# Performance work log

Measured on AMD Instinct MI355X. Metric: run time of the kernel, lower is better.

## Reference

```python
import jax, jax.numpy as jnp
import numpy as np

SR = 16000
NYQ = SR / 2.0
N_FFT = 400
HOP = 160
WIN = 400
OUT_CHANNELS = 64
OUTPUT_SIZE = 64
MIN_LOW_HZ = 50.0
MIN_BAND_HZ = 50.0
FRAME_LENGTH = 400
EPS_LN = 1e-5


def _to_mel(hz):
    return 2595.0 * np.log10(1.0 + hz / 700.0)


def _to_hz(mel):
    return 700.0 * (10.0 ** (mel / 2595.0) - 1.0)


def setup_inputs() -> dict:
    key = jax.random.key(0)
    k1, = jax.random.split(key, 1)
    waveforms = jax.random.normal(k1, (1024, 1, 16000), dtype=jnp.float32)
    # mel-spaced init, exactly as in __init__ (freq_init='mel', range_constraint=False)
    low_hz = 30.0
    high_hz = NYQ - (MIN_LOW_HZ + MIN_BAND_HZ)
    mel = np.linspace(_to_mel(low_hz), _to_mel(high_hz), OUT_CHANNELS + 1)
    hz = _to_hz(mel)
    low_hz_ = jnp.asarray(hz[:-1], dtype=jnp.float32).reshape(-1, 1)
    band_hz_ = jnp.asarray(np.diff(hz), dtype=jnp.float32).reshape(-1, 1)
    ln_weight = jnp.ones((OUT_CHANNELS, 1), dtype=jnp.float32)
    ln_bias = jnp.zeros((OUT_CHANNELS, 1), dtype=jnp.float32)
    return {
        "waveforms": waveforms,
        "low_hz_": low_hz_,
        "band_hz_": band_hz_,
        "ln_weight": ln_weight,
        "ln_bias": ln_bias,
    }


def _hann_periodic(n):
    # torch.hann_window default: periodic=True
    k = jnp.arange(n, dtype=jnp.float32)
    return 0.5 - 0.5 * jnp.cos(2.0 * jnp.pi * k / n)


def _stft_mag(x):
    pad = N_FFT // 2
    xp = jnp.pad(x, ((0, 0), (pad, pad)), mode="reflect")
    n_frames = 1 + (xp.shape[1] - N_FFT) // HOP
    idx = jnp.arange(n_frames)[:, None] * HOP + jnp.arange(N_FFT)[None, :]
    frames = xp[:, idx] * _hann_periodic(WIN)  # [B, F_t, n_fft]
    spec = jnp.fft.rfft(frames, axis=-1)       # [B, F_t, n_fft//2+1]
    return jnp.abs(spec).transpose(0, 2, 1)    # [B, n_fft//2+1, F_t]


def _get_filters(low_hz_, band_hz_):
    # vectorized over all channels (original loops per channel)
    low = MIN_LOW_HZ + jnp.abs(low_hz_)                                   # [C,1]
    high = jnp.clip(low + MIN_BAND_HZ + jnp.abs(band_hz_), MIN_LOW_HZ, NYQ)
    freq = jnp.linspace(0.0, NYQ, N_FFT // 2 + 1, dtype=jnp.float32)      # [F]
    mask = (freq >= low) & (freq <= high)                                 # [C,F]
    center = (low + high) / 2.0
    bw = high - low
    resp = 1.0 - jnp.abs(freq - center) / (bw / 2.0)                      # triangular
    return jnp.where(mask, resp, 0.0)                                     # [C,F]


def _gln(x, weight, bias):
    # GlobalLayerNorm over dims (1,2) of [B,C,T]
    mean = jnp.mean(x, axis=(1, 2), keepdims=True)
    var = jnp.mean((x - mean) ** 2, axis=(1, 2), keepdims=True)
    return weight * (x - mean) / jnp.sqrt(var + EPS_LN) + bias


def _interp_linear(x, out_size):
    # torch F.interpolate(mode='linear', align_corners=False) along last dim
    t_in = x.shape[-1]
    scale = t_in / out_size
    pos = (jnp.arange(out_size, dtype=jnp.float32) + 0.5) * scale - 0.5
    pos = jnp.clip(pos, 0.0, t_in - 1)
    i0 = jnp.floor(pos).astype(jnp.int32)
    i1 = jnp.minimum(i0 + 1, t_in - 1)
    w = (pos - i0.astype(jnp.float32))
    return x[..., i0] * (1.0 - w) + x[..., i1] * w


def reference(waveforms, low_hz_, band_hz_, ln_weight, ln_bias):
    B = waveforms.shape[0]
    target_length = HOP * (OUTPUT_SIZE - 1) + FRAME_LENGTH  # 10480
    cur = waveforms.shape[-1]
    x = waveforms[:, 0, :]
    if target_length > cur:  # static shape decision
        x = jnp.pad(x, ((0, 0), (0, target_length - cur)))
    mag_spec = _stft_mag(x)                       # [B, 201, F_t]
    filters = _get_filters(low_hz_, band_hz_)     # [C, 201]
    filtered = jnp.einsum("cf,bft->bct", filters, mag_spec)  # [B, C, F_t]
    filtered = _gln(filtered, ln_weight, ln_bias)
    energy = filtered ** 2
    log_energy = jnp.log10(energy + 1e-6)         # [B, C, F_t]
    if log_energy.shape[-1] != OUTPUT_SIZE:
        log_energy = _interp_linear(log_energy, OUTPUT_SIZE)  # [B, C, 64]
    log_energy = log_energy[:, None, :, :].transpose(0, 1, 3, 2)  # [B,1,64,C]
    return (log_energy, filters)
```

## Files before the change

### kernel.cpp

```cpp
#include <hip/hip_runtime.h>
#include <math.h>

#define BLOCK 512
#define MSTR 209

typedef __attribute__((ext_vector_type(8))) short short8;
typedef __attribute__((ext_vector_type(16))) float f32x16;
typedef __attribute__((ext_vector_type(8))) float f32x8;

__device__ inline unsigned short f2bf(float x) {
    unsigned u = __float_as_uint(x);
    unsigned r = u + 0x7fffu + ((u >> 16) & 1u);
    return (unsigned short)(r >> 16);
}

struct ASplit { short8 h, l; };

__device__ inline ASplit splitA(f32x8 v) {
    unsigned ah[4], al[4];
    #pragma unroll
    for (int q = 0; q < 4; ++q) {
        unsigned short h0 = f2bf(v[2*q]),   h1 = f2bf(v[2*q+1]);
        float hf0 = __uint_as_float((unsigned)h0 << 16);
        float hf1 = __uint_as_float((unsigned)h1 << 16);
        unsigned short l0 = f2bf(v[2*q] - hf0), l1 = f2bf(v[2*q+1] - hf1);
        ah[q] = (unsigned)h0 | ((unsigned)h1 << 16);
        al[q] = (unsigned)l0 | ((unsigned)l1 << 16);
    }
    ASplit r;
    r.h = __builtin_bit_cast(short8, *(uint4*)ah);
    r.l = __builtin_bit_cast(short8, *(uint4*)al);
    return r;
}

__device__ inline f32x8 loadA8(const float* __restrict__ x, int i0) {
    f32x8 r;
    if (i0 >= 0 && i0 <= 15992) {
        float4 a0 = *(const float4*)(x + i0);
        float4 a1 = *(const float4*)(x + i0 + 4);
        r[0] = a0.x; r[1] = a0.y; r[2] = a0.z; r[3] = a0.w;
        r[4] = a1.x; r[5] = a1.y; r[6] = a1.z; r[7] = a1.w;
    } else {
        #pragma unroll
        for (int e = 0; e < 8; ++e) {
            int p = i0 + e;
            p = (p < 0) ? -p : p;
            p = (p > 15999) ? (31998 - p) : p;
            r[e] = x[p];
        }
    }
    return r;
}

__global__ void fse_filters(const float* __restrict__ low_hz_,
                            const float* __restrict__ band_hz_,
                            float* __restrict__ out)
{
    int idx = blockIdx.x * 256 + threadIdx.x;
    if (idx >= 64 * 201) return;
    int c = idx / 201;
    int k = idx - c * 201;
    float lo = 50.0f + fabsf(low_hz_[c]);
    float hi = lo + 50.0f + fabsf(band_hz_[c]);
    hi = fminf(fmaxf(hi, 50.0f), 8000.0f);
    float ctr = 0.5f * (lo + hi);
    float hbw = 0.5f * (hi - lo);
    float fq = 40.0f * (float)k;
    float resp = 1.0f - fabsf(fq - ctr) / hbw;
    out[idx] = (fq >= lo && fq <= hi) ? resp : 0.0f;
}

__global__ void fse_setup_B(unsigned short* __restrict__ bt)
{
    int idx = blockIdx.x * 256 + threadIdx.x;
    if (idx >= 372736) return;
    int e   = idx & 7;
    int t   = idx >> 3;
    int row = t % 448;
    int q   = t / 448;
    int p   = q & 3;
    int pl  = (q >> 2) & 1;
    int kc  = q >> 3;
    int n   = kc * 32 + p * 8 + e;
    float v = 0.0f;
    if (n < 400) {
        int bin = -1, isim = 0;
        if (row <= 200) bin = row;
        else if (row >= 224 && row <= 424) { bin = row - 224; isim = 1; }
        if (bin >= 0) {
            int a = (bin * n) % 400;
            float th = 6.283185307179586f * ((float)a / 400.0f);
            float sn, cs;
            sincosf(th, &sn, &cs);
            float wn = 0.5f - 0.5f * cosf(6.283185307179586f * ((float)n / 400.0f));
            v = isim ? (-wn * sn) : (wn * cs);
        }
    }
    unsigned short h = f2bf(v);
    float hf = __uint_as_float((unsigned)h << 16);
    unsigned short l = f2bf(v - hf);
    bt[idx] = pl ? l : h;
}

__global__ __launch_bounds__(512, 2)
void fse_main_mfma(const float* __restrict__ wav,
                   const float* __restrict__ low_hz_,
                   const float* __restrict__ band_hz_,
                   const float* __restrict__ ln_w,
                   const float* __restrict__ ln_b,
                   const unsigned short* __restrict__ Bt,
                   float* __restrict__ out)
{
    __shared__ __align__(16) char smem[114688];
    float* mags = (float*)smem;
    float* fbuf = (float*)(smem + 84544);

    __shared__ float fctr[64], finv[64];
    __shared__ int   fks[64], fke[64];
    __shared__ float red[16];
    __shared__ float stats[2];

    const int b    = blockIdx.x;
    const int tid  = threadIdx.x;
    const int w    = tid >> 6;
    const int lane = tid & 63;
    const float* __restrict__ x = wav + b * 16000;

    if (tid < 64) {
        float lo = 50.0f + fabsf(low_hz_[tid]);
        float hi = lo + 50.0f + fabsf(band_hz_[tid]);
        hi = fminf(fmaxf(hi, 50.0f), 8000.0f);
        float ctr = 0.5f * (lo + hi);
        float hbw = 0.5f * (hi - lo);
        int ks = (int)ceilf(lo * 0.025f);
        if (ks < 0) ks = 0;
        while (40.0f * (float)ks < lo) ++ks;
        while (ks > 0 && 40.0f * (float)(ks - 1) >= lo) --ks;
        int ke = (int)floorf(hi * 0.025f);
        if (ke > 200) ke = 200;
        while (40.0f * (float)ke > hi) --ke;
        while (ke < 200 && 40.0f * (float)(ke + 1) <= hi) ++ke;
        fctr[tid] = ctr;
        finv[tid] = (hbw > 0.0f) ? (1.0f / hbw) : 0.0f;
        fks[tid]  = ks;
        fke[tid]  = ke;
    }

    const int mt   = w >> 1;
    const int half = w & 1;
    const int jrow = lane & 31;
    const int g    = lane >> 5;
    const int arow = mt * 32 + jrow;
    const int te   = (arow <= 100) ? arow : 50;
    const int abase = 160 * te - 200 + g * 8;

    const uint4* __restrict__ btg = (const uint4*)Bt;

    f32x8 ac0 = loadA8(x, abase);
    f32x8 ac1 = loadA8(x, abase + 16);
    {
        uint4 rr0 = btg[0 * 512 + tid], rr1 = btg[1 * 512 + tid];
        uint4 rr2 = btg[2 * 512 + tid], rr3 = btg[3 * 512 + tid];
        uint4 rr4 = btg[4 * 512 + tid], rr5 = btg[5 * 512 + tid];
        uint4 rr6 = btg[6 * 512 + tid];
        uint4* dst = (uint4*)smem;
        dst[0 * 512 + tid] = rr0; dst[1 * 512 + tid] = rr1;
        dst[2 * 512 + tid] = rr2; dst[3 * 512 + tid] = rr3;
        dst[4 * 512 + tid] = rr4; dst[5 * 512 + tid] = rr5;
        dst[6 * 512 + tid] = rr6;
    }
    __syncthreads();

    f32x16 acc[7];
    #pragma unroll
    for (int n = 0; n < 7; ++n) {
        #pragma unroll
        for (int e = 0; e < 16; ++e) acc[n][e] = 0.0f;
    }

    int curoff = 0;
    for (int kc = 0; kc < 13; ++kc) {
        const bool pre = (kc < 12);
        uint4 rr0, rr1, rr2, rr3, rr4, rr5, rr6;
        f32x8 an0, an1;
        if (pre) {
            const uint4* src = btg + (kc + 1) * 3584;
            rr0 = src[0 * 512 + tid]; rr1 = src[1 * 512 + tid];
            rr2 = src[2 * 512 + tid]; rr3 = src[3 * 512 + tid];
            rr4 = src[4 * 512 + tid]; rr5 = src[5 * 512 + tid];
            rr6 = src[6 * 512 + tid];
            an0 = loadA8(x, abase + (kc + 1) * 32);
            an1 = loadA8(x, abase + (kc + 1) * 32 + 16);
        }

        ASplit A0 = splitA(ac0);
        ASplit A1 = splitA(ac1);

        const unsigned short* bs = (const unsigned short*)(smem + curoff);
        #pragma unroll
        for (int s = 0; s < 2; ++s) {
            const short8 Ah = s ? A1.h : A0.h;
            const short8 Al = s ? A1.l : A0.l;
            const int pb = (s * 2 + g) * 448;
            #pragma unroll
            for (int n = 0; n < 7; ++n) {
                const int ro = (half * 7 + n) * 32 + jrow;
                short8 Bh = *(const short8*)(bs + (pb + ro) * 8);
                short8 Bl = *(const short8*)(bs + 14336 + (pb + ro) * 8);
                acc[n] = __builtin_amdgcn_mfma_f32_32x32x16_bf16(Ah, Bh, acc[n], 0, 0, 0);
                acc[n] = __builtin_amdgcn_mfma_f32_32x32x16_bf16(Ah, Bl, acc[n], 0, 0, 0);
                acc[n] = __builtin_amdgcn_mfma_f32_32x32x16_bf16(Al, Bh, acc[n], 0, 0, 0);
            }
        }

        if (pre) {
            uint4* dst = (uint4*)(smem + (curoff ^ 57344));
            dst[0 * 512 + tid] = rr0; dst[1 * 512 + tid] = rr1;
            dst[2 * 512 + tid] = rr2; dst[3 * 512 + tid] = rr3;
            dst[4 * 512 + tid] = rr4; dst[5 * 512 + tid] = rr5;
            dst[6 * 512 + tid] = rr6;
        }
        __syncthreads();
        if (pre) { ac0 = an0; ac1 = an1; }
        curoff ^= 57344;
    }

    if (half == 0) {
        #pragma unroll
        for (int n = 0; n < 7; ++n) {
            int k = n * 32 + jrow;
            if (k <= 200) {
                #pragma unroll
                for (int r = 0; r < 16; ++r) {
                    int t = mt * 32 + (r & 3) + 8 * (r >> 2) + 4 * g;
                    if (t <= 100) mags[t * MSTR + k] = acc[n][r];
                }
            }
        }
    }
    __syncthreads();
    if (half == 1) {
        #pragma unroll
        for (int n = 0; n < 7; ++n) {
            int k = n * 32 + jrow;
            if (k <= 200) {
                #pragma unroll
                for (int r = 0; r < 16; ++r) {
                    int t = mt * 32 + (r & 3) + 8 * (r >> 2) + 4 * g;
                    if (t <= 100) {
                        float re = mags[t * MSTR + k];
                        float im = acc[n][r];
                        mags[t * MSTR + k] = sqrtf(re * re + im * im);
                    }
                }
            }
        }
    }
    __syncthreads();

    {
        const int t0 = lane;
        const int t1v = 64 + lane;
        const int t1 = (t1v <= 100) ? t1v : 100;
        #pragma unroll
        for (int i = 0; i < 8; ++i) {
            const int c = w * 8 + i;
            const float ctr = fctr[c];
            const float inv = finv[c];
            const int ks = fks[c], ke = fke[c];
            float a0 = 0.0f, a1 = 0.0f;
            for (int k = ks; k <= ke; ++k) {
                float resp = 1.0f - fabsf(40.0f * (float)k - ctr) * inv;
                a0 = fmaf(resp, mags[t0 * MSTR + k], a0);
                a1 = fmaf(resp, mags[t1 * MSTR + k], a1);
            }
            fbuf[c * 101 + t0] = a0;
            if (t1v <= 100) fbuf[c * 101 + t1v] = a1;
        }
    }
    __syncthreads();

    float s = 0.0f, ss = 0.0f;
    for (int i = tid; i < 6464; i += BLOCK) {
        float vv = fbuf[i];
        s += vv;
        ss = fmaf(vv, vv, ss);
    }
    #pragma unroll
    for (int off = 32; off > 0; off >>= 1) {
        s  += __shfl_down(s,  off, 64);
        ss += __shfl_down(ss, off, 64);
    }
    if (lane == 0) { red[w] = s; red[8 + w] = ss; }
    __syncthreads();
    if (tid == 0) {
        float ts = 0.0f, tss = 0.0f;
        for (int i = 0; i < 8; ++i) { ts += red[i]; tss += red[8 + i]; }
        float mu = ts * (1.0f / 6464.0f);
        stats[0] = mu;
        stats[1] = tss * (1.0f / 6464.0f) - mu * mu;
    }
    __syncthreads();
    const float mu   = stats[0];
    const float isig = 1.0f / sqrtf(stats[1] + 1e-5f);

    for (int idx = tid; idx < 4096; idx += BLOCK) {
        const int to = idx >> 6;
        const int c  = idx & 63;
        float pos = ((float)to + 0.5f) * 1.578125f - 0.5f;
        pos = fminf(fmaxf(pos, 0.0f), 100.0f);
        int i0 = (int)floorf(pos);
        int i1 = i0 + 1; if (i1 > 100) i1 = 100;
        float fr = pos - (float)i0;
        float wc = ln_w[c], bc = ln_b[c];
        float x0 = fbuf[c * 101 + i0];
        float x1 = fbuf[c * 101 + i1];
        float y0 = fmaf(wc, (x0 - mu) * isig, bc);
        float y1 = fmaf(wc, (x1 - mu) * isig, bc);
        float l0 = log10f(fmaf(y0, y0, 1e-6f));
        float l1 = log10f(fmaf(y1, y1, 1e-6f));
        out[b * 4096 + idx] = l0 * (1.0f - fr) + l1 * fr;
    }
}

__global__ __launch_bounds__(512, 2)
void fse_main_valu(const float* __restrict__ wav,
                   const float* __restrict__ low_hz_,
                   const float* __restrict__ band_hz_,
                   const float* __restrict__ ln_w,
                   const float* __restrict__ ln_b,
                   float* __restrict__ out)
{
    __shared__ float  xp[16400];
    __shared__ float2 Xs[8][204];
    __shared__ float  mags[8][204];
    __shared__ float  fbuf[64 * 101];
    __shared__ float  fctr[64], finv[64];
    __shared__ int    fks[64], fke[64];
    __shared__ float  red[8];
    __shared__ float  stats[2];

    const int b    = blockIdx.x;
    const int tid  = threadIdx.x;
    const int w    = tid >> 6;
    const int lane = tid & 63;
    const float* __restrict__ x = wav + b * 16000;

    for (int i = tid; i < 16400; i += BLOCK) {
        int p = i - 200;
        p = (p < 0) ? -p : p;
        p = (p > 15999) ? (31998 - p) : p;
        xp[i] = x[p];
    }
    if (tid < 64) {
        float lo = 50.0f + fabsf(low_hz_[tid]);
        float hi = lo + 50.0f + fabsf(band_hz_[tid]);
        hi = fminf(fmaxf(hi, 50.0f), 8000.0f);
        float ctr = 0.5f * (lo + hi);
        float hbw = 0.5f * (hi - lo);
        int ks = (int)ceilf(lo * 0.025f);
        if (ks < 0) ks = 0;
        while (40.0f * (float)ks < lo) ++ks;
        while (ks > 0 && 40.0f * (float)(ks - 1) >= lo) --ks;
        int ke = (int)floorf(hi * 0.025f);
        if (ke > 200) ke = 200;
        while (40.0f * (float)ke > hi) --ke;
        while (ke < 200 && 40.0f * (float)(ke + 1) <= hi) ++ke;
        fctr[tid] = ctr;
        finv[tid] = (hbw > 0.0f) ? (1.0f / hbw) : 0.0f;
        fks[tid]  = ks;
        fke[tid]  = ke;
    }
    __syncthreads();

    const float cctr = fctr[lane];
    const float cinv = finv[lane];
    const int   cks  = fks[lane];
    const int   cke  = fke[lane];

    float reX[4][13], imX[4][13];
    const float2* __restrict__ xp2 = (const float2*)xp;
    float c0[4], s0[4], c1[4], s1[4], cd[4], sd[4];
    #pragma unroll
    for (int m = 0; m < 4; ++m) {
        const int k = m * 64 + lane;
        const float th = -0.015707963267948966f * (float)k;
        sincosf(th, &s1[m], &c1[m]);
        sincosf(th + th, &sd[m], &cd[m]);
        c0[m] = 1.0f; s0[m] = 0.0f;
        #pragma unroll
        for (int j = 0; j < 13; ++j) { reX[m][j] = 0.0f; imX[m][j] = 0.0f; }
    }
    const int o12 = (w < 5) ? 640 * 12 : 0;
    int ib = 80 * w;
    #pragma unroll 2
    for (int h = 0; h < 200; ++h) {
        #pragma unroll
        for (int j = 0; j < 13; ++j) {
            const int off = (j == 12) ? o12 : 640 * j;
            float2 f = xp2[ib + off];
            #pragma unroll
            for (int m = 0; m < 4; ++m) {
                reX[m][j] = fmaf(f.x, c0[m], reX[m][j]);
                imX[m][j] = fmaf(f.x, s0[m], imX[m][j]);
                reX[m][j] = fmaf(f.y, c1[m], reX[m][j]);
                imX[m][j] = fmaf(f.y, s1[m], imX[m][j]);
            }
        }
        #pragma unroll
        for (int m = 0; m < 4; ++m) {
            float nc0 = fmaf(c0[m], cd[m], -(s0[m] * sd[m]));
            float ns0 = fmaf(s0[m], cd[m],  (c0[m] * sd[m]));
            float nc1 = fmaf(c1[m], cd[m], -(s1[m] * sd[m]));
            float ns1 = fmaf(s1[m], cd[m],  (c1[m] * sd[m]));
            c0[m] = nc0; s0[m] = ns0; c1[m] = nc1; s1[m] = ns1;
        }
        ++ib;
    }

    float2* __restrict__ myX   = &Xs[w][0];
    float*  __restrict__ mymag = &mags[w][0];
    for (int j = 0; j < 13; ++j) {
        const int t = w + 8 * j;
        if (t > 100) break;
        #pragma unroll
        for (int m = 0; m < 4; ++m) {
            const int k = m * 64 + lane;
            if (k < 202) myX[k] = make_float2(reX[m][j], imX[m][j]);
        }
        asm volatile("s_waitcnt lgkmcnt(0)" ::: "memory");
        #pragma unroll
        for (int m = 0; m < 4; ++m) {
            const int k = m * 64 + lane;
            if (k <= 200) {
                float2 xm = (k == 0) ? myX[1] : myX[k - 1];
                float imm = (k == 0) ? -xm.y : xm.y;
                float2 xq = myX[k + 1];
                float rw = 0.5f * reX[m][j] - 0.25f * (xm.x + xq.x);
                float iw = 0.5f * imX[m][j] - 0.25f * (imm  + xq.y);
                mymag[k] = sqrtf(rw * rw + iw * iw);
            }
        }
        asm volatile("s_waitcnt lgkmcnt(0)" ::: "memory");
        float acc = 0.0f;
        for (int k = cks; k <= cke; ++k) {
            float resp = 1.0f - fabsf(40.0f * (float)k - cctr) * cinv;
            acc = fmaf(resp, mymag[k], acc);
        }
        fbuf[lane * 101 + t] = acc;
    }
    __syncthreads();

    float s = 0.0f;
    for (int i = tid; i < 6464; i += BLOCK) s += fbuf[i];
    #pragma unroll
    for (int off = 32; off > 0; off >>= 1) s += __shfl_down(s, off, 64);
    if (lane == 0) red[w] = s;
    __syncthreads();
    if (tid == 0) {
        float tsum = 0.0f;
        for (int i = 0; i < 8; ++i) tsum += red[i];
        stats[0] = tsum * (1.0f / 6464.0f);
    }
    __syncthreads();
    const float mu = stats[0];
    float v = 0.0f;
    for (int i = tid; i < 6464; i += BLOCK) { float d = fbuf[i] - mu; v = fmaf(d, d, v); }
    #pragma unroll
    for (int off = 32; off > 0; off >>= 1) v += __shfl_down(v, off, 64);
    if (lane == 0) red[w] = v;
    __syncthreads();
    if (tid == 0) {
        float tsum = 0.0f;
        for (int i = 0; i < 8; ++i) tsum += red[i];
        stats[1] = tsum * (1.0f / 6464.0f);
    }
    __syncthreads();
    const float var  = stats[1];
    const float isig = 1.0f / sqrtf(var + 1e-5f);

    for (int idx = tid; idx < 4096; idx += BLOCK) {
        const int to = idx >> 6;
        const int c  = idx & 63;
        float pos = ((float)to + 0.5f) * 1.578125f - 0.5f;
        pos = fminf(fmaxf(pos, 0.0f), 100.0f);
        int i0 = (int)floorf(pos);
        int i1 = i0 + 1; if (i1 > 100) i1 = 100;
        float fr = pos - (float)i0;
        float wc = ln_w[c], bc = ln_b[c];
        float x0 = fbuf[c * 101 + i0];
        float x1 = fbuf[c * 101 + i1];
        float y0 = fmaf(wc, (x0 - mu) * isig, bc);
        float y1 = fmaf(wc, (x1 - mu) * isig, bc);
        float l0 = log10f(fmaf(y0, y0, 1e-6f));
        float l1 = log10f(fmaf(y1, y1, 1e-6f));
        out[b * 4096 + idx] = l0 * (1.0f - fr) + l1 * fr;
    }
}

extern "C" void kernel_launch(void* const* d_in, const int* in_sizes, int n_in,
                              void* d_out, int out_size, void* d_ws, size_t ws_size,
                              hipStream_t stream)
{
    const float* wav = (const float*)d_in[0];
    const float* lo  = (const float*)d_in[1];
    const float* bd  = (const float*)d_in[2];
    const float* lw  = (const float*)d_in[3];
    const float* lb  = (const float*)d_in[4];
    float* out = (float*)d_out;

    fse_filters<<<(64 * 201 + 255) / 256, 256, 0, stream>>>(lo, bd, out + 1024 * 4096);

    const size_t BNEED = (size_t)372736 * sizeof(unsigned short);
    if (ws_size >= BNEED) {
        unsigned short* Bts = (unsigned short*)d_ws;
        fse_setup_B<<<(372736 + 255) / 256, 256, 0, stream>>>(Bts);
        fse_main_mfma<<<1024, BLOCK, 0, stream>>>(wav, lo, bd, lw, lb, Bts, out);
    } else {
        fse_main_valu<<<1024, BLOCK, 0, stream>>>(wav, lo, bd, lw, lb, out);
    }
}
```

Baseline: 231.7 us.

## Split fused STFT kernel into per-half-batch GEMM kernel and separate layernorm kernel

The single per-batch fused kernel becomes two kernels. A GEMM kernel runs two blocks per batch element, each covering half the time frames, stages B tiles into LDS with global_load_lds instead of register-staged double buffering, computes real and imaginary parts in the same wave so magnitude needs no LDS round trip, and writes filtered energies to workspace. A second kernel then does layernorm, log, and interpolation. The aim is to raise occupancy (lower LDS per block, 4 blocks per CU) and parallelism, at the cost of an extra global round trip for the intermediate, an extra launch, and dropping the prefetch overlap. The VALU fallback path is removed, and the fused MFMA kernel is kept as the fallback when workspace is small.

Result: slower. 249.7 us (+7.8%).

```diff
diff --git a/kernel.cpp b/kernel.cpp
--- a/kernel.cpp
+++ b/kernel.cpp
@@ -1,8 +1,5 @@
 #include <hip/hip_runtime.h>
 #include <math.h>
-
-#define BLOCK 512
-#define MSTR 209
 
 typedef __attribute__((ext_vector_type(8))) short short8;
 typedef __attribute__((ext_vector_type(16))) float f32x16;
@@ -50,6 +47,27 @@
         }
     }
     return r;
+}
+
+__device__ inline void filter_params(int c, const float* low_hz_, const float* band_hz_,
+                                     float* fctr, float* finv, int* fks, int* fke) {
+    float lo = 50.0f + fabsf(low_hz_[c]);
+    float hi = lo + 50.0f + fabsf(band_hz_[c]);
+    hi = fminf(fmaxf(hi, 50.0f), 8000.0f);
+    float ctr = 0.5f * (lo + hi);
+    float hbw = 0.5f * (hi - lo);
+    int ks = (int)ceilf(lo * 0.025f);
+    if (ks < 0) ks = 0;
+    while (40.0f * (float)ks < lo) ++ks;
+    while (ks > 0 && 40.0f * (float)(ks - 1) >= lo) --ks;
+    int ke = (int)floorf(hi * 0.025f);
+    if (ke > 200) ke = 200;
+    while (40.0f * (float)ke > hi) --ke;
+    while (ke < 200 && 40.0f * (float)(ke + 1) <= hi) ++ke;
+    fctr[c] = ctr;
+    finv[c] = (hbw > 0.0f) ? (1.0f / hbw) : 0.0f;
+    fks[c]  = ks;
+    fke[c]  = ke;
 }
 
 __global__ void fse_filters(const float* __restrict__ low_hz_,
@@ -102,200 +120,158 @@
     bt[idx] = pl ? l : h;
 }
 
-__global__ __launch_bounds__(512, 2)
-void fse_main_mfma(const float* __restrict__ wav,
-                   const float* __restrict__ low_hz_,
-                   const float* __restrict__ band_hz_,
-                   const float* __restrict__ ln_w,
-                   const float* __restrict__ ln_b,
-                   const unsigned short* __restrict__ Bt,
-                   float* __restrict__ out)
+__global__ __launch_bounds__(512, 4)
+void fse_gemm(const float* __restrict__ wav,
+              const float* __restrict__ low_hz_,
+              const float* __restrict__ band_hz_,
+              const unsigned short* __restrict__ Bt,
+              float* __restrict__ filt)
 {
-    __shared__ __align__(16) char smem[114688];
-    float* mags = (float*)smem;
-    float* fbuf = (float*)(smem + 84544);
-
+    __shared__ __align__(16) char smem[57344];
     __shared__ float fctr[64], finv[64];
     __shared__ int   fks[64], fke[64];
-    __shared__ float red[16];
+    float* mags = (float*)smem;
+
+    const int bid  = blockIdx.x;
+    const int b    = bid >> 1;
+    const int half = bid & 1;
+    const int tid  = threadIdx.x;
+    const int w    = tid >> 6;
+    const int lane = tid & 63;
+    const float* __restrict__ x = wav + b * 16000;
+
+    if (tid < 64) filter_params(tid, low_hz_, band_hz_, fctr, finv, fks, fke);
+
+    const int mt    = w >> 2;
+    const int pq    = w & 3;
+    const int pbase = pq * 2;
+    const int cnt   = (pq < 3) ? 2 : 1;
+    const int jrow  = lane & 31;
+    const int g     = lane >> 5;
+
+    const int arow = 64 * half + 32 * mt + jrow;
+    const int te   = (arow <= 100) ? arow : 50;
+    const int ab   = 160 * te - 200 + g * 8;
+
+    f32x16 accR[2], accI[2];
+    #pragma unroll
+    for (int i = 0; i < 2; ++i)
+        #pragma unroll
+        for (int e = 0; e < 16; ++e) { accR[i][e] = 0.0f; accI[i][e] = 0.0f; }
+
+    for (int kc = 0; kc < 13; ++kc) {
+        __syncthreads();
+        {
+            const uint4* src = (const uint4*)Bt + kc * 3584 + (w << 6) + lane;
+            char* dstb = smem + (w << 6) * 16;
+            #pragma unroll
+            for (int i = 0; i < 7; ++i) {
+                __builtin_amdgcn_global_load_lds(
+                    (const __attribute__((address_space(1))) unsigned*)(src + i * 512),
+                    (__attribute__((address_space(3))) unsigned*)(dstb + i * 8192),
+                    16, 0, 0);
+            }
+        }
+        __syncthreads();
+
+        f32x8 a0 = loadA8(x, ab + kc * 32);
+        f32x8 a1 = loadA8(x, ab + kc * 32 + 16);
+
+        const unsigned short* bs = (const unsigned short*)smem;
+        #pragma unroll
+        for (int s = 0; s < 2; ++s) {
+            ASplit S = splitA(s ? a1 : a0);
+            const int part = s * 2 + g;
+            const int bhof = part * 3584;
+            const int blof = (4 + part) * 3584;
+            #pragma unroll
+            for (int i = 0; i < 2; ++i) {
+                if (i < cnt) {
+                    const int p = pbase + i;
+                    const int roR = p * 32 + jrow;
+                    const int roI = (p + 7) * 32 + jrow;
+                    short8 BhR = *(const short8*)(bs + bhof + roR * 8);
+                    short8 BlR = *(const short8*)(bs + blof + roR * 8);
+                    short8 BhI = *(const short8*)(bs + bhof + roI * 8);
+                    short8 BlI = *(const short8*)(bs + blof + roI * 8);
+                    accR[i] = __builtin_amdgcn_mfma_f32_32x32x16_bf16(S.h, BhR, accR[i], 0, 0, 0);
+                    accR[i] = __builtin_amdgcn_mfma_f32_32x32x16_bf16(S.h, BlR, accR[i], 0, 0, 0);
+                    accR[i] = __builtin_amdgcn_mfma_f32_32x32x16_bf16(S.l, BhR, accR[i], 0, 0, 0);
+                    accI[i] = __builtin_amdgcn_mfma_f32_32x32x16_bf16(S.h, BhI, accI[i], 0, 0, 0);
+                    accI[i] = __builtin_amdgcn_mfma_f32_32x32x16_bf16(S.h, BlI, accI[i], 0, 0, 0);
+                    accI[i] = __builtin_amdgcn_mfma_f32_32x32x16_bf16(S.l, BhI, accI[i], 0, 0, 0);
+                }
+            }
+        }
+    }
+
+    __syncthreads();
+
+    #pragma unroll
+    for (int i = 0; i < 2; ++i) {
+        if (i < cnt) {
+            const int k = (pbase + i) * 32 + jrow;
+            if (k <= 200) {
+                #pragma unroll
+                for (int r = 0; r < 16; ++r) {
+                    int tl = 32 * mt + (r & 3) + 8 * (r >> 2) + 4 * g;
+                    float re = accR[i][r];
+                    float im = accI[i][r];
+                    mags[tl * 201 + k] = sqrtf(re * re + im * im);
+                }
+            }
+        }
+    }
+    __syncthreads();
+
+    const int tg = 64 * half + lane;
+    #pragma unroll
+    for (int i = 0; i < 8; ++i) {
+        const int c = w * 8 + i;
+        const float ctr = fctr[c];
+        const float inv = finv[c];
+        const int ks = fks[c], ke = fke[c];
+        float a = 0.0f;
+        for (int k = ks; k <= ke; ++k) {
+            float resp = 1.0f - fabsf(40.0f * (float)k - ctr) * inv;
+            a = fmaf(resp, mags[lane * 201 + k], a);
+        }
+        if (tg <= 100) filt[b * 6464 + c * 101 + tg] = a;
+    }
+}
+
+__global__ __launch_bounds__(256)
+void fse_post(const float* __restrict__ filt,
+              const float* __restrict__ ln_w,
+              const float* __restrict__ ln_b,
+              float* __restrict__ out)
+{
+    __shared__ float fbuf[6464];
+    __shared__ float red[8];
     __shared__ float stats[2];
-
     const int b    = blockIdx.x;
     const int tid  = threadIdx.x;
     const int w    = tid >> 6;
     const int lane = tid & 63;
-    const float* __restrict__ x = wav + b * 16000;
-
-    if (tid < 64) {
-        float lo = 50.0f + fabsf(low_hz_[tid]);
-        float hi = lo + 50.0f + fabsf(band_hz_[tid]);
-        hi = fminf(fmaxf(hi, 50.0f), 8000.0f);
-        float ctr = 0.5f * (lo + hi);
-        float hbw = 0.5f * (hi - lo);
-        int ks = (int)ceilf(lo * 0.025f);
-        if (ks < 0) ks = 0;
-        while (40.0f * (float)ks < lo) ++ks;
-        while (ks > 0 && 40.0f * (float)(ks - 1) >= lo) --ks;
-        int ke = (int)floorf(hi * 0.025f);
-        if (ke > 200) ke = 200;
-        while (40.0f * (float)ke > hi) --ke;
-        while (ke < 200 && 40.0f * (float)(ke + 1) <= hi) ++ke;
-        fctr[tid] = ctr;
-        finv[tid] = (hbw > 0.0f) ? (1.0f / hbw) : 0.0f;
-        fks[tid]  = ks;
-        fke[tid]  = ke;
-    }
-
-    const int mt   = w >> 1;
-    const int half = w & 1;
-    const int jrow = lane & 31;
-    const int g    = lane >> 5;
-    const int arow = mt * 32 + jrow;
-    const int te   = (arow <= 100) ? arow : 50;
-    const int abase = 160 * te - 200 + g * 8;
-
-    const uint4* __restrict__ btg = (const uint4*)Bt;
-
-    f32x8 ac0 = loadA8(x, abase);
-    f32x8 ac1 = loadA8(x, abase + 16);
-    {
-        uint4 rr0 = btg[0 * 512 + tid], rr1 = btg[1 * 512 + tid];
-        uint4 rr2 = btg[2 * 512 + tid], rr3 = btg[3 * 512 + tid];
-        uint4 rr4 = btg[4 * 512 + tid], rr5 = btg[5 * 512 + tid];
-        uint4 rr6 = btg[6 * 512 + tid];
-        uint4* dst = (uint4*)smem;
-        dst[0 * 512 + tid] = rr0; dst[1 * 512 + tid] = rr1;
-        dst[2 * 512 + tid] = rr2; dst[3 * 512 + tid] = rr3;
-        dst[4 * 512 + tid] = rr4; dst[5 * 512 + tid] = rr5;
-        dst[6 * 512 + tid] = rr6;
-    }
-    __syncthreads();
-
-    f32x16 acc[7];
-    #pragma unroll
-    for (int n = 0; n < 7; ++n) {
-        #pragma unroll
-        for (int e = 0; e < 16; ++e) acc[n][e] = 0.0f;
-    }
-
-    int curoff = 0;
-    for (int kc = 0; kc < 13; ++kc) {
-        const bool pre = (kc < 12);
-        uint4 rr0, rr1, rr2, rr3, rr4, rr5, rr6;
-        f32x8 an0, an1;
-        if (pre) {
-            const uint4* src = btg + (kc + 1) * 3584;
-            rr0 = src[0 * 512 + tid]; rr1 = src[1 * 512 + tid];
-            rr2 = src[2 * 512 + tid]; rr3 = src[3 * 512 + tid];
-            rr4 = src[4 * 512 + tid]; rr5 = src[5 * 512 + tid];
-            rr6 = src[6 * 512 + tid];
-            an0 = loadA8(x, abase + (kc + 1) * 32);
-            an1 = loadA8(x, abase + (kc + 1) * 32 + 16);
-        }
-
-        ASplit A0 = splitA(ac0);
-        ASplit A1 = splitA(ac1);
-
-        const unsigned short* bs = (const unsigned short*)(smem + curoff);
-        #pragma unroll
-        for (int s = 0; s < 2; ++s) {
-            const short8 Ah = s ? A1.h : A0.h;
-            const short8 Al = s ? A1.l : A0.l;
-            const int pb = (s * 2 + g) * 448;
-            #pragma unroll
-            for (int n = 0; n < 7; ++n) {
-                const int ro = (half * 7 + n) * 32 + jrow;
-                short8 Bh = *(const short8*)(bs + (pb + ro) * 8);
-                short8 Bl = *(const short8*)(bs + 14336 + (pb + ro) * 8);
-                acc[n] = __builtin_amdgcn_mfma_f32_32x32x16_bf16(Ah, Bh, acc[n], 0, 0, 0);
-                acc[n] = __builtin_amdgcn_mfma_f32_32x32x16_bf16(Ah, Bl, acc[n], 0, 0, 0);
-                acc[n] = __builtin_amdgcn_mfma_f32_32x32x16_bf16(Al, Bh, acc[n], 0, 0, 0);
-            }
-        }
-
-        if (pre) {
-            uint4* dst = (uint4*)(smem + (curoff ^ 57344));
-            dst[0 * 512 + tid] = rr0; dst[1 * 512 + tid] = rr1;
-            dst[2 * 512 + tid] = rr2; dst[3 * 512 + tid] = rr3;
-            dst[4 * 512 + tid] = rr4; dst[5 * 512 + tid] = rr5;
-            dst[6 * 512 + tid] = rr6;
-        }
-        __syncthreads();
-        if (pre) { ac0 = an0; ac1 = an1; }
-        curoff ^= 57344;
-    }
-
-    if (half == 0) {
-        #pragma unroll
-        for (int n = 0; n < 7; ++n) {
-            int k = n * 32 + jrow;
-            if (k <= 200) {
-                #pragma unroll
-                for (int r = 0; r < 16; ++r) {
-                    int t = mt * 32 + (r & 3) + 8 * (r >> 2) + 4 * g;
-                    if (t <= 100) mags[t * MSTR + k] = acc[n][r];
-                }
-            }
-        }
-    }
-    __syncthreads();
-    if (half == 1) {
-        #pragma unroll
-        for (int n = 0; n < 7; ++n) {
-            int k = n * 32 + jrow;
-            if (k <= 200) {
-                #pragma unroll
-                for (int r = 0; r < 16; ++r) {
-                    int t = mt * 32 + (r & 3) + 8 * (r >> 2) + 4 * g;
-                    if (t <= 100) {
-                        float re = mags[t * MSTR + k];
-                        float im = acc[n][r];
-                        mags[t * MSTR + k] = sqrtf(re * re + im * im);
-                    }
-                }
-            }
-        }
-    }
-    __syncthreads();
-
-    {
-        const int t0 = lane;
-        const int t1v = 64 + lane;
-        const int t1 = (t1v <= 100) ? t1v : 100;
-        #pragma unroll
-        for (int i = 0; i < 8; ++i) {
-            const int c = w * 8 + i;
-            const float ctr = fctr[c];
-            const float inv = finv[c];
-            const int ks = fks[c], ke = fke[c];
-            float a0 = 0.0f, a1 = 0.0f;
-            for (int k = ks; k <= ke; ++k) {
-                float resp = 1.0f - fabsf(40.0f * (float)k - ctr) * inv;
-                a0 = fmaf(resp, mags[t0 * MSTR + k], a0);
-                a1 = fmaf(resp, mags[t1 * MSTR + k], a1);
-            }
-            fbuf[c * 101 + t0] = a0;
-            if (t1v <= 100) fbuf[c * 101 + t1v] = a1;
-        }
-    }
-    __syncthreads();
+    const float* __restrict__ src = filt + b * 6464;
 
     float s = 0.0f, ss = 0.0f;
-    for (int i = tid; i < 6464; i += BLOCK) {
-        float vv = fbuf[i];
-        s += vv;
-        ss = fmaf(vv, vv, ss);
+    for (int i = tid; i < 6464; i += 256) {
+        float v = src[i];
+        fbuf[i] = v;
+        s += v;
+        ss = fmaf(v, v, ss);
     }
     #pragma unroll
     for (int off = 32; off > 0; off >>= 1) {
         s  += __shfl_down(s,  off, 64);
         ss += __shfl_down(ss, off, 64);
     }
-    if (lane == 0) { red[w] = s; red[8 + w] = ss; }
+    if (lane == 0) { red[w] = s; red[4 + w] = ss; }
     __syncthreads();
     if (tid == 0) {
         float ts = 0.0f, tss = 0.0f;
-        for (int i = 0; i < 8; ++i) { ts += red[i]; tss += red[8 + i]; }
+        for (int i = 0; i < 4; ++i) { ts += red[i]; tss += red[4 + i]; }
         float mu = ts * (1.0f / 6464.0f);
         stats[0] = mu;
         stats[1] = tss * (1.0f / 6464.0f) - mu * mu;
@@ -304,7 +280,7 @@
     const float mu   = stats[0];
     const float isig = 1.0f / sqrtf(stats[1] + 1e-5f);
 
-    for (int idx = tid; idx < 4096; idx += BLOCK) {
+    for (int idx = tid; idx < 4096; idx += 256) {
         const int to = idx >> 6;
         const int c  = idx & 63;
         float pos = ((float)to + 0.5f) * 1.578125f - 0.5f;
@@ -323,22 +299,23 @@
     }
 }
 
+#define MSTR 209
 __global__ __launch_bounds__(512, 2)
-void fse_main_valu(const float* __restrict__ wav,
-                   const float* __restrict__ low_hz_,
-                   const float* __restrict__ band_hz_,
-                   const float* __restrict__ ln_w,
-                   const float* __restrict__ ln_b,
-                   float* __restrict__ out)
+void fse_main_fused(const float* __restrict__ wav,
+                    const float* __restrict__ low_hz_,
+                    const float* __restrict__ band_hz_,
+                    const float* __restrict__ ln_w,
+                    const float* __restrict__ ln_b,
+                    const unsigned short* __restrict__ Bt,
+                    float* __restrict__ out)
 {
-    __shared__ float  xp[16400];
-    __shared__ float2 Xs[8][204];
-    __shared__ float  mags[8][204];
-    __shared__ float  fbuf[64 * 101];
-    __shared__ float  fctr[64], finv[64];
-    __shared__ int    fks[64], fke[64];
-    __shared__ float  red[8];
-    __shared__ float  stats[2];
+    __shared__ __align__(16) char smem[114688];
+    float* mags = (float*)smem;
+    float* fbuf = (float*)(smem + 84544);
+    __shared__ float fctr[64], finv[64];
+    __shared__ int   fks[64], fke[64];
+    __shared__ float red[16];
+    __shared__ float stats[2];
 
     const int b    = blockIdx.x;
     const int tid  = threadIdx.x;
@@ -346,140 +323,164 @@
     const int lane = tid & 63;
     const float* __restrict__ x = wav + b * 16000;
 
-    for (int i = tid; i < 16400; i += BLOCK) {
-        int p = i - 200;
-        p = (p < 0) ? -p : p;
-        p = (p > 15999) ? (31998 - p) : p;
-        xp[i] = x[p];
-    }
-    if (tid < 64) {
-        float lo = 50.0f + fabsf(low_hz_[tid]);
-        float hi = lo + 50.0f + fabsf(band_hz_[tid]);
-        hi = fminf(fmaxf(hi, 50.0f), 8000.0f);
-        float ctr = 0.5f * (lo + hi);
-        float hbw = 0.5f * (hi - lo);
-        int ks = (int)ceilf(lo * 0.025f);
-        if (ks < 0) ks = 0;
-        while (40.0f * (float)ks < lo) ++ks;
-        while (ks > 0 && 40.0f * (float)(ks - 1) >= lo) --ks;
-        int ke = (int)floorf(hi * 0.025f);
-        if (ke > 200) ke = 200;
-        while (40.0f * (float)ke > hi) --ke;
-        while (ke < 200 && 40.0f * (float)(ke + 1) <= hi) ++ke;
-        fctr[tid] = ctr;
-        finv[tid] = (hbw > 0.0f) ? (1.0f / hbw) : 0.0f;
-        fks[tid]  = ks;
-        fke[tid]  = ke;
-    }
-    __syncthreads();
-
-    const float cctr = fctr[lane];
-    const float cinv = finv[lane];
-    const int   cks  = fks[lane];
-    const int   cke  = fke[lane];
-
-    float reX[4][13], imX[4][13];
-    const float2* __restrict__ xp2 = (const float2*)xp;
-    float c0[4], s0[4], c1[4], s1[4], cd[4], sd[4];
-    #pragma unroll
-    for (int m = 0; m < 4; ++m) {
-        const int k = m * 64 + lane;
-        const float th = -0.015707963267948966f * (float)k;
-        sincosf(th, &s1[m], &c1[m]);
-        sincosf(th + th, &sd[m], &cd[m]);
-        c0[m] = 1.0f; s0[m] = 0.0f;
-        #pragma unroll
-        for (int j = 0; j < 13; ++j) { reX[m][j] = 0.0f; imX[m][j] = 0.0f; }
-    }
-    const int o12 = (w < 5) ? 640 * 12 : 0;
-    int ib = 80 * w;
-    #pragma unroll 2
-    for (int h = 0; h < 200; ++h) {
-        #pragma unroll
-        for (int j = 0; j < 13; ++j) {
-            const int off = (j == 12) ? o12 : 640 * j;
-            float2 f = xp2[ib + off];
+    if (tid < 64) filter_params(tid, low_hz_, band_hz_, fctr, finv, fks, fke);
+
+    const int mt   = w >> 1;
+    const int half = w & 1;
+    const int jrow = lane & 31;
+    const int g    = lane >> 5;
+    const int arow = mt * 32 + jrow;
+    const int te   = (arow <= 100) ? arow : 50;
+    const int abase = 160 * te - 200 + g * 8;
+
+    const uint4* __restrict__ btg = (const uint4*)Bt;
+
+    f32x8 ac0 = loadA8(x, abase);
+    f32x8 ac1 = loadA8(x, abase + 16);
+    {
+        uint4 rr0 = btg[0 * 512 + tid], rr1 = btg[1 * 512 + tid];
+        uint4 rr2 = btg[2 * 512 + tid], rr3 = btg[3 * 512 + tid];
+        uint4 rr4 = btg[4 * 512 + tid], rr5 = btg[5 * 512 + tid];
+        uint4 rr6 = btg[6 * 512 + tid];
+        uint4* dst = (uint4*)smem;
+        dst[0 * 512 + tid] = rr0; dst[1 * 512 + tid] = rr1;
+        dst[2 * 512 + tid] = rr2; dst[3 * 512 + tid] = rr3;
+        dst[4 * 512 + tid] = rr4; dst[5 * 512 + tid] = rr5;
+        dst[6 * 512 + tid] = rr6;
+    }
+    __syncthreads();
+
+    f32x16 acc[7];
+    #pragma unroll
+    for (int n = 0; n < 7; ++n)
+        #pragma unroll
+        for (int e = 0; e < 16; ++e) acc[n][e] = 0.0f;
+
+    int curoff = 0;
+    for (int kc = 0; kc < 13; ++kc) {
+        const bool pre = (kc < 12);
+        uint4 rr0, rr1, rr2, rr3, rr4, rr5, rr6;
+        f32x8 an0, an1;
+        if (pre) {
+            const uint4* src = btg + (kc + 1) * 3584;
+            rr0 = src[0 * 512 + tid]; rr1 = src[1 * 512 + tid];
+            rr2 = src[2 * 512 + tid]; rr3 = src[3 * 512 + tid];
+            rr4 = src[4 * 512 + tid]; rr5 = src[5 * 512 + tid];
+            rr6 = src[6 * 512 + tid];
+            an0 = loadA8(x, abase + (kc + 1) * 32);
+            an1 = loadA8(x, abase + (kc + 1) * 32 + 16);
+        }
+        ASplit A0 = splitA(ac0);
+        ASplit A1 = splitA(ac1);
+
+        const unsigned short* bs = (const unsigned short*)(smem + curoff);
+        #pragma unroll
+        for (int s = 0; s < 2; ++s) {
+            const short8 Ah = s ? A1.h : A0.h;
+            const short8 Al = s ? A1.l : A0.l;
+            const int pb = (s * 2 + g) * 448;
             #pragma unroll
-            for (int m = 0; m < 4; ++m) {
-                reX[m][j] = fmaf(f.x, c0[m], reX[m][j]);
-                imX[m][j] = fmaf(f.x, s0[m], imX[m][j]);
-                reX[m][j] = fmaf(f.y, c1[m], reX[m][j]);
-                imX[m][j] = fmaf(f.y, s1[m], imX[m][j]);
-            }
-        }
-        #pragma unroll
-        for (int m = 0; m < 4; ++m) {
-            float nc0 = fmaf(c0[m], cd[m], -(s0[m] * sd[m]));
-            float ns0 = fmaf(s0[m], cd[m],  (c0[m] * sd[m]));
-            float nc1 = fmaf(c1[m], cd[m], -(s1[m] * sd[m]));
-            float ns1 = fmaf(s1[m], cd[m],  (c1[m] * sd[m]));
-            c0[m] = nc0; s0[m] = ns0; c1[m] = nc1; s1[m] = ns1;
-        }
-        ++ib;
-    }
-
-    float2* __restrict__ myX   = &Xs[w][0];
-    float*  __restrict__ mymag = &mags[w][0];
-    for (int j = 0; j < 13; ++j) {
-        const int t = w + 8 * j;
-        if (t > 100) break;
-        #pragma unroll
-        for (int m = 0; m < 4; ++m) {
-            const int k = m * 64 + lane;
-            if (k < 202) myX[k] = make_float2(reX[m][j], imX[m][j]);
-        }
-        asm volatile("s_waitcnt lgkmcnt(0)" ::: "memory");
-        #pragma unroll
-        for (int m = 0; m < 4; ++m) {
-            const int k = m * 64 + lane;
+            for (int n = 0; n < 7; ++n) {
+                const int ro = (half * 7 + n) * 32 + jrow;
+                short8 Bh = *(const short8*)(bs + (pb + ro) * 8);
+                short8 Bl = *(const short8*)(bs + 14336 + (pb + ro) * 8);
+                acc[n] = __builtin_amdgcn_mfma_f32_32x32x16_bf16(Ah, Bh, acc[n], 0, 0, 0);
+                acc[n] = __builtin_amdgcn_mfma_f32_32x32x16_bf16(Ah, Bl, acc[n], 0, 0, 0);
+                acc[n] = __builtin_amdgcn_mfma_f32_32x32x16_bf16(Al, Bh, acc[n], 0, 0, 0);
+            }
+        }
+        if (pre) {
+            uint4* dst = (uint4*)(smem + (curoff ^ 57344));
+            dst[0 * 512 + tid] = rr0; dst[1 * 512 + tid] = rr1;
+            dst[2 * 512 + tid] = rr2; dst[3 * 512 + tid] = rr3;
+            dst[4 * 512 + tid] = rr4; dst[5 * 512 + tid] = rr5;
+            dst[6 * 512 + tid] = rr6;
+        }
+        __syncthreads();
+        if (pre) { ac0 = an0; ac1 = an1; }
+        curoff ^= 57344;
+    }
+
+    if (half == 0) {
+        #pragma unroll
+        for (int n = 0; n < 7; ++n) {
+            int k = n * 32 + jrow;
             if (k <= 200) {
-                float2 xm = (k == 0) ? myX[1] : myX[k - 1];
-                float imm = (k == 0) ? -xm.y : xm.y;
-                float2 xq = myX[k + 1];
-                float rw = 0.5f * reX[m][j] - 0.25f * (xm.x + xq.x);
-                float iw = 0.5f * imX[m][j] - 0.25f * (imm  + xq.y);
-                mymag[k] = sqrtf(rw * rw + iw * iw);
-            }
-        }
-        asm volatile("s_waitcnt lgkmcnt(0)" ::: "memory");
-        float acc = 0.0f;
-        for (int k = cks; k <= cke; ++k) {
-            float resp = 1.0f - fabsf(40.0f * (float)k - cctr) * cinv;
-            acc = fmaf(resp, mymag[k], acc);
-        }
-        fbuf[lane * 101 + t] = acc;
-    }
-    __syncthreads();
-
-    float s = 0.0f;
-    for (int i = tid; i < 6464; i += BLOCK) s += fbuf[i];
-    #pragma unroll
-    for (int off = 32; off > 0; off >>= 1) s += __shfl_down(s, off, 64);
-    if (lane == 0) red[w] = s;
+                #pragma unroll
+                for (int r = 0; r < 16; ++r) {
+                    int t = mt * 32 + (r & 3) + 8 * (r >> 2) + 4 * g;
+                    if (t <= 100) mags[t * MSTR + k] = acc[n][r];
+                }
+            }
+        }
+    }
+    __syncthreads();
+    if (half == 1) {
+        #pragma unroll
+        for (int n = 0; n < 7; ++n) {
+            int k = n * 32 + jrow;
+            if (k <= 200) {
+                #pragma unroll
+                for (int r = 0; r < 16; ++r) {
+                    int t = mt * 32 + (r & 3) + 8 * (r >> 2) + 4 * g;
+                    if (t <= 100) {
+                        float re = mags[t * MSTR + k];
+                        float im = acc[n][r];
+                        mags[t * MSTR + k] = sqrtf(re * re + im * im);
+                    }
+                }
+            }
+        }
+    }
+    __syncthreads();
+
+    {
+        const int t0 = lane;
+        const int t1v = 64 + lane;
+        const int t1 = (t1v <= 100) ? t1v : 100;
+        #pragma unroll
+        for (int i = 0; i < 8; ++i) {
+            const int c = w * 8 + i;
+            const float ctr = fctr[c];
+            const float inv = finv[c];
+            const int ks = fks[c], ke = fke[c];
+            float a0 = 0.0f, a1 = 0.0f;
+            for (int k = ks; k <= ke; ++k) {
+                float resp = 1.0f - fabsf(40.0f * (float)k - ctr) * inv;
+                a0 = fmaf(resp, mags[t0 * MSTR + k], a0);
+                a1 = fmaf(resp, mags[t1 * MSTR + k], a1);
+            }
+            fbuf[c * 101 + t0] = a0;
+            if (t1v <= 100) fbuf[c * 101 + t1v] = a1;
+        }
+    }
+    __syncthreads();
+
+    float s = 0.0f, ss = 0.0f;
+    for (int i = tid; i < 6464; i += 512) {
+        float vv = fbuf[i];
+        s += vv;
+        ss = fmaf(vv, vv, ss);
+    }
+    #pragma unroll
+    for (int off = 32; off > 0; off >>= 1) {
+        s  += __shfl_down(s,  off, 64);
+        ss += __shfl_down(ss, off, 64);
+    }
+    if (lane == 0) { red[w] = s; red[8 + w] = ss; }
     __syncthreads();
     if (tid == 0) {
-        float tsum = 0.0f;
-        for (int i = 0; i < 8; ++i) tsum += red[i];
-        stats[0] = tsum * (1.0f / 6464.0f);
-    }
-    __syncthreads();
-    const float mu = stats[0];
-    float v = 0.0f;
-    for (int i = tid; i < 6464; i += BLOCK) { float d = fbuf[i] - mu; v = fmaf(d, d, v); }
-    #pragma unroll
-    for (int off = 32; off > 0; off >>= 1) v += __shfl_down(v, off, 64);
-    if (lane == 0) red[w] = v;
-    __syncthreads();
-    if (tid == 0) {
-        float tsum = 0.0f;
-        for (int i = 0; i < 8; ++i) tsum += red[i];
-        stats[1] = tsum * (1.0f / 6464.0f);
-    }
-    __syncthreads();
-    const float var  = stats[1];
-    const float isig = 1.0f / sqrtf(var + 1e-5f);
-
-    for (int idx = tid; idx < 4096; idx += BLOCK) {
+        float ts = 0.0f, tss = 0.0f;
+        for (int i = 0; i < 8; ++i) { ts += red[i]; tss += red[8 + i]; }
+        float mu = ts * (1.0f / 6464.0f);
+        stats[0] = mu;
+        stats[1] = tss * (1.0f / 6464.0f) - mu * mu;
+    }
+    __syncthreads();
+    const float mu   = stats[0];
+    const float isig = 1.0f / sqrtf(stats[1] + 1e-5f);
+
+    for (int idx = tid; idx < 4096; idx += 512) {
         const int to = idx >> 6;
         const int c  = idx & 63;
         float pos = ((float)to + 0.5f) * 1.578125f - 0.5f;
@@ -511,12 +512,16 @@
 
     fse_filters<<<(64 * 201 + 255) / 256, 256, 0, stream>>>(lo, bd, out + 1024 * 4096);
 
-    const size_t BNEED = (size_t)372736 * sizeof(unsigned short);
-    if (ws_size >= BNEED) {
-        unsigned short* Bts = (unsigned short*)d_ws;
-        fse_setup_B<<<(372736 + 255) / 256, 256, 0, stream>>>(Bts);
-        fse_main_mfma<<<1024, BLOCK, 0, stream>>>(wav, lo, bd, lw, lb, Bts, out);
+    const size_t BN1 = 745472;
+    const size_t BN2 = BN1 + (size_t)1024 * 6464 * 4;
+    unsigned short* Bts = (unsigned short*)d_ws;
+    fse_setup_B<<<(372736 + 255) / 256, 256, 0, stream>>>(Bts);
+
+    if (ws_size >= BN2) {
+        float* filt = (float*)((char*)d_ws + BN1);
+        fse_gemm<<<2048, 512, 0, stream>>>(wav, lo, bd, Bts, filt);
+        fse_post<<<1024, 256, 0, stream>>>(filt, lw, lb, out);
     } else {
-        fse_main_valu<<<1024, BLOCK, 0, stream>>>(wav, lo, bd, lw, lb, out);
-    }
-}
+        fse_main_fused<<<1024, 512, 0, stream>>>(wav, lo, bd, lw, lb, Bts, out);
+    }
+}
```
